# Kernel optimization log

Measured on AMD Instinct MI355X. Metric: run time of the kernel, lower is better.

The kernel has to match this reference:

```python
import jax, jax.numpy as jnp
import numpy as np

B, FMAX, H, LF, LC = 512, 16, 128, 64, 256
TAU, BIAS = 1000000.0, 1.0


def _gru(x, W_ih, W_hh, b_ih, b_hh):
    # x: [N, L, H]; torch GRU gate order (r, z, n)
    def step(h, xt):
        gi = xt @ W_ih.T + b_ih            # [N, 3H]
        gh = h @ W_hh.T + b_hh
        ir, iz, in_ = jnp.split(gi, 3, axis=-1)
        hr, hz, hn = jnp.split(gh, 3, axis=-1)
        r = jax.nn.sigmoid(ir + hr)
        z = jax.nn.sigmoid(iz + hz)
        n = jnp.tanh(in_ + r * hn)
        h_new = (1.0 - z) * n + z * h
        return h_new, h_new
    h0 = jnp.zeros((x.shape[0], W_hh.shape[1]), x.dtype)
    _, hs = jax.lax.scan(step, h0, jnp.swapaxes(x, 0, 1))
    return jnp.swapaxes(hs, 0, 1)          # [N, L, H]


def setup_inputs() -> dict:
    key = jax.random.key(0)
    ks = jax.random.split(key, 12)
    counts = (np.arange(B) % FMAX) + 1      # group sizes, max == FMAX
    N = int(counts.sum())                   # 4352
    user_idx = np.repeat(np.arange(B), counts).astype(np.int32)
    offsets = np.concatenate([[0], np.cumsum(counts)])
    gather_idx = np.zeros((B, FMAX), np.int32)
    pad_mask = np.zeros((B, FMAX), np.int32)
    for b in range(B):
        c = counts[b]
        gather_idx[b, :c] = offsets[b] + np.arange(c)
        pad_mask[b, :c] = 1
    lf = (np.arange(N) % LF) + 1
    friend_src_mask = (np.arange(LF)[None, :] < lf[:, None]).astype(np.int32)
    lc = (np.arange(N) % LC) + 1
    common_src_mask = (np.arange(LC)[None, :] < lc[:, None]).astype(np.int32)
    s = 1.0 / np.sqrt(H)
    return {
        "self_x": jax.random.normal(ks[0], (B, H), jnp.float32),
        "common_x": jax.random.normal(ks[1], (N, LC, H), jnp.float32),
        "common_time": jax.random.uniform(ks[2], (N, LC), jnp.float32) * 1e6,
        "friend_x": jax.random.normal(ks[3], (N, LF, H), jnp.float32),
        "W_ih": jax.random.uniform(ks[4], (3 * H, H), jnp.float32, -s, s),
        "W_hh": jax.random.uniform(ks[5], (3 * H, H), jnp.float32, -s, s),
        "b_ih": jax.random.uniform(ks[6], (3 * H,), jnp.float32, -s, s),
        "b_hh": jax.random.uniform(ks[7], (3 * H,), jnp.float32, -s, s),
        "W_friend": jax.random.uniform(ks[8], (H, 2 * H), jnp.float32, -s, s),
        "W_beta": jax.random.uniform(ks[9], (H, H), jnp.float32, -s, s),
        "friend_src_mask": jnp.asarray(friend_src_mask),
        "common_src_mask": jnp.asarray(common_src_mask),
        "user_idx": jnp.asarray(user_idx),
        "gather_idx": jnp.asarray(gather_idx),
        "pad_mask": jnp.asarray(pad_mask),
    }


def reference(self_x, common_x, common_time, friend_x, W_ih, W_hh, b_ih, b_hh,
              W_friend, W_beta, friend_src_mask, common_src_mask, user_idx,
              gather_idx, pad_mask):
    # --- FRIENDRNN: GRU encode, take last valid step per friend ---
    hs = _gru(friend_x, W_ih, W_hh, b_ih, b_hh)                 # [N, LF, H]
    fmask = friend_src_mask.astype(hs.dtype)
    hs = hs * fmask[..., None]
    idx_last = (friend_src_mask.sum(axis=1) - 1).astype(jnp.int32)  # [N]
    friend_out = jnp.take_along_axis(hs, idx_last[:, None, None], axis=1)[:, 0, :]  # [N, H]

    # --- FRIENDSHIP: temporal-decayed content attention over common items ---
    self_rep = self_x[user_idx]                                  # [N, H]
    sf = jnp.concatenate([self_rep, friend_out], axis=-1) @ W_friend.T  # [N, H]
    proj_common = common_x @ W_beta.T                            # [N, LC, H]
    scores = jnp.einsum('nlh,nh->nl', proj_common, sf)           # [N, LC]
    content = jax.nn.softplus(scores)
    temporal = jnp.exp(-common_time / TAU + BIAS)
    tf = jnp.sum(content * temporal * common_src_mask.astype(content.dtype), axis=-1)  # [N]

    # --- pad to groups (zeros, matching pad_sequence), softmax-weighted agg ---
    pm = pad_mask.astype(tf.dtype)                               # [B, FMAX]
    tf_pad = tf[gather_idx] * pm                                 # [B, FMAX]
    fx_pad = friend_out[gather_idx] * pm[..., None]              # [B, FMAX, H]
    w = jax.nn.softmax(tf_pad, axis=-1)                          # over padded zeros too (faithful)
    return jnp.sum(w[..., None] * fx_pad, axis=1)                # [B, H]
```

## Files before the change

kernel.cpp:

```cpp
#include <hip/hip_runtime.h>
#include <hip/hip_bf16.h>

typedef float float4v __attribute__((ext_vector_type(4)));
typedef __bf16 bf16x8 __attribute__((ext_vector_type(8)));

#define MFMA16(a, b, c) __builtin_amdgcn_mfma_f32_16x16x32_bf16(a, b, c, 0, 0, 0)

__device__ __forceinline__ float fsigmoid(float x) {
    return __builtin_amdgcn_rcpf(1.0f + __expf(-x));
}
__device__ __forceinline__ float ftanh_(float x) {
    float e = __expf(2.0f * x);
    return 1.0f - 2.0f * __builtin_amdgcn_rcpf(e + 1.0f);
}
__device__ __forceinline__ float softplusf(float x) {
    return fmaxf(x, 0.0f) + __logf(1.0f + __expf(-fabsf(x)));
}

__global__ __launch_bounds__(256, 1)
void gru_kernel(const float* __restrict__ friend_x,
                const float* __restrict__ W_ih, const float* __restrict__ W_hh,
                const float* __restrict__ b_ih, const float* __restrict__ b_hh,
                const int* __restrict__ fmask,
                float* __restrict__ friend_out)
{
    __shared__ __align__(16) __bf16 lds[8 * 2048];
    __shared__ int s_lf[16];
    __shared__ int s_n[16];

    const int tid = threadIdx.x;
    const int wv = tid >> 6;
    const int lane = tid & 63;
    const int cn = lane & 15;
    const int qq = lane >> 4;

    __bf16* const XH0 = lds;
    __bf16* const XH1 = lds + 2048;
    __bf16* const XL0 = lds + 2 * 2048;
    __bf16* const XL1 = lds + 3 * 2048;
    __bf16* const HH0 = lds + 4 * 2048;
    __bf16* const HH1 = lds + 5 * 2048;
    __bf16* const HL0 = lds + 6 * 2048;
    __bf16* const HL1 = lds + 7 * 2048;

    if (tid < 16) {
        const int p = blockIdx.x * 16 + tid;
        const int v = p / 68;
        const int j = p - v * 68;
        const int n = (63 - v) + 64 * j;
        s_n[tid] = n;
        const int* mp = fmask + (long)n * 64;
        int s = 0;
        for (int i = 0; i < 64; ++i) s += mp[i];
        s_lf[tid] = s;
    }

    {
        bf16x8 z8;
#pragma unroll
        for (int j = 0; j < 8; ++j) z8[j] = (__bf16)0.0f;
        for (int i = tid; i < 4 * 2048 / 8; i += 256) ((bf16x8*)HH0)[i] = z8;
    }

    bf16x8 wihh[3][2][4], wihl[3][2][4], whhh[3][2][4], whhl[3][2][4];
#pragma unroll
    for (int gate = 0; gate < 3; ++gate)
#pragma unroll
        for (int ct = 0; ct < 2; ++ct) {
            const int row = gate * 128 + wv * 32 + ct * 16 + cn;
#pragma unroll
            for (int c = 0; c < 4; ++c) {
                const float* p = W_ih + row * 128 + c * 32 + qq * 8;
                float4v u0 = *(const float4v*)p;
                float4v u1 = *(const float4v*)(p + 4);
                bf16x8 fh, fl;
#pragma unroll
                for (int j = 0; j < 4; ++j) {
                    __bf16 h0 = (__bf16)u0[j]; fh[j] = h0; fl[j] = (__bf16)(u0[j] - (float)h0);
                    __bf16 h1 = (__bf16)u1[j]; fh[j + 4] = h1; fl[j + 4] = (__bf16)(u1[j] - (float)h1);
                }
                wihh[gate][ct][c] = fh; wihl[gate][ct][c] = fl;
                const float* q = W_hh + row * 128 + c * 32 + qq * 8;
                float4v v0 = *(const float4v*)q;
                float4v v1 = *(const float4v*)(q + 4);
                bf16x8 gh, gl;
#pragma unroll
                for (int j = 0; j < 4; ++j) {
                    __bf16 h0 = (__bf16)v0[j]; gh[j] = h0; gl[j] = (__bf16)(v0[j] - (float)h0);
                    __bf16 h1 = (__bf16)v1[j]; gh[j + 4] = h1; gl[j + 4] = (__bf16)(v1[j] - (float)h1);
                }
                whhh[gate][ct][c] = gh; whhl[gate][ct][c] = gl;
            }
        }

    float biasR[2], biasZ[2], biasIN[2], biasHN[2];
#pragma unroll
    for (int ct = 0; ct < 2; ++ct) {
        const int cc = wv * 32 + ct * 16 + cn;
        biasR[ct] = b_ih[cc] + b_hh[cc];
        biasZ[ct] = b_ih[128 + cc] + b_hh[128 + cc];
        biasIN[ct] = b_ih[256 + cc];
        biasHN[ct] = b_hh[256 + cc];
    }

    __syncthreads();

    const int srow = lane & 15;
    const int ss = lane >> 4;
    const float* xp = friend_x + (long)s_n[srow] * 8192 + wv * 32 + ss * 8;

    int lfA[4], nA[4];
#pragma unroll
    for (int r = 0; r < 4; ++r) { lfA[r] = s_lf[qq * 4 + r]; nA[r] = s_n[qq * 4 + r]; }
    int maxlf = 0;
    for (int i = 0; i < 16; ++i) maxlf = (s_lf[i] > maxlf) ? s_lf[i] : maxlf;

    {
        float4v u0 = *(const float4v*)(xp);
        float4v u1 = *(const float4v*)(xp + 4);
        bf16x8 fh, fl;
#pragma unroll
        for (int j = 0; j < 4; ++j) {
            __bf16 h0 = (__bf16)u0[j]; fh[j] = h0; fl[j] = (__bf16)(u0[j] - (float)h0);
            __bf16 h1 = (__bf16)u1[j]; fh[j + 4] = h1; fl[j + 4] = (__bf16)(u1[j] - (float)h1);
        }
        *(bf16x8*)&XH0[tid * 8] = fh;
        *(bf16x8*)&XL0[tid * 8] = fl;
    }
    __syncthreads();

    float hC[2][4];
#pragma unroll
    for (int ct = 0; ct < 2; ++ct)
#pragma unroll
        for (int r = 0; r < 4; ++r) hC[ct][r] = 0.0f;

    for (int t = 0; t < maxlf; ++t) {
        const int cur = t & 1;
        __bf16* const XHc = cur ? XH1 : XH0;
        __bf16* const XLc = cur ? XL1 : XL0;
        __bf16* const HHc = cur ? HH1 : HH0;
        __bf16* const HLc = cur ? HL1 : HL0;
        __bf16* const XHn = cur ? XH0 : XH1;
        __bf16* const XLn = cur ? XL0 : XL1;
        __bf16* const HHn = cur ? HH0 : HH1;
        __bf16* const HLn = cur ? HL0 : HL1;
        const bool pf = (t + 1 < maxlf);

        float4v u0, u1;
        if (pf) {
            u0 = *(const float4v*)(xp + (t + 1) * 128);
            u1 = *(const float4v*)(xp + (t + 1) * 128 + 4);
        }

        float4v aR[2], aZ[2], aIN[2], aHN[2];
#pragma unroll
        for (int ct = 0; ct < 2; ++ct) {
            aR[ct] = (float4v){biasR[ct], biasR[ct], biasR[ct], biasR[ct]};
            aZ[ct] = (float4v){biasZ[ct], biasZ[ct], biasZ[ct], biasZ[ct]};
            aIN[ct] = (float4v){biasIN[ct], biasIN[ct], biasIN[ct], biasIN[ct]};
            aHN[ct] = (float4v){biasHN[ct], biasHN[ct], biasHN[ct], biasHN[ct]};
        }

#pragma unroll
        for (int c = 0; c < 4; ++c) {
            const int fo_ = (c * 64 + lane) * 8;
            bf16x8 xh = *(const bf16x8*)&XHc[fo_];
            bf16x8 xl = *(const bf16x8*)&XLc[fo_];
            bf16x8 hh = *(const bf16x8*)&HHc[fo_];
            bf16x8 hl = *(const bf16x8*)&HLc[fo_];
#pragma unroll
            for (int ct = 0; ct < 2; ++ct) {
                aR[ct] = MFMA16(xh, wihh[0][ct][c], aR[ct]);
                aR[ct] = MFMA16(xl, wihh[0][ct][c], aR[ct]);
                aR[ct] = MFMA16(xh, wihl[0][ct][c], aR[ct]);
                aR[ct] = MFMA16(hh, whhh[0][ct][c], aR[ct]);
                aR[ct] = MFMA16(hl, whhh[0][ct][c], aR[ct]);
                aR[ct] = MFMA16(hh, whhl[0][ct][c], aR[ct]);

                aZ[ct] = MFMA16(xh, wihh[1][ct][c], aZ[ct]);
                aZ[ct] = MFMA16(xl, wihh[1][ct][c], aZ[ct]);
                aZ[ct] = MFMA16(xh, wihl[1][ct][c], aZ[ct]);
                aZ[ct] = MFMA16(hh, whhh[1][ct][c], aZ[ct]);
                aZ[ct] = MFMA16(hl, whhh[1][ct][c], aZ[ct]);
                aZ[ct] = MFMA16(hh, whhl[1][ct][c], aZ[ct]);

                aIN[ct] = MFMA16(xh, wihh[2][ct][c], aIN[ct]);
                aIN[ct] = MFMA16(xl, wihh[2][ct][c], aIN[ct]);
                aIN[ct] = MFMA16(xh, wihl[2][ct][c], aIN[ct]);

                aHN[ct] = MFMA16(hh, whhh[2][ct][c], aHN[ct]);
                aHN[ct] = MFMA16(hl, whhh[2][ct][c], aHN[ct]);
                aHN[ct] = MFMA16(hh, whhl[2][ct][c], aHN[ct]);
            }
        }

#pragma unroll
        for (int ct = 0; ct < 2; ++ct) {
            const int col = wv * 32 + ct * 16 + cn;
            const int c2 = col >> 5, s2 = (col >> 3) & 3, j2 = col & 7;
#pragma unroll
            for (int reg = 0; reg < 4; ++reg) {
                const int row = qq * 4 + reg;
                float r = fsigmoid(aR[ct][reg]);
                float z = fsigmoid(aZ[ct][reg]);
                float nn = ftanh_(aIN[ct][reg] + r * aHN[ct][reg]);
                float h = (1.0f - z) * nn + z * hC[ct][reg];
                hC[ct][reg] = h;
                __bf16 hhi = (__bf16)h;
                __bf16 hlo = (__bf16)(h - (float)hhi);
                const int sl = (c2 * 64 + row + 16 * s2) * 8 + j2;
                HHn[sl] = hhi;
                HLn[sl] = hlo;
                if (t + 1 == lfA[reg])
                    friend_out[(long)nA[reg] * 128 + col] = h;
            }
        }

        if (pf) {
            bf16x8 fh, fl;
#pragma unroll
            for (int j = 0; j < 4; ++j) {
                __bf16 h0 = (__bf16)u0[j]; fh[j] = h0; fl[j] = (__bf16)(u0[j] - (float)h0);
                __bf16 h1 = (__bf16)u1[j]; fh[j + 4] = h1; fl[j + 4] = (__bf16)(u1[j] - (float)h1);
            }
            *(bf16x8*)&XHn[tid * 8] = fh;
            *(bf16x8*)&XLn[tid * 8] = fl;
        }
        __syncthreads();
    }
}

__global__ __launch_bounds__(256)
void attn_kernel(const float* __restrict__ self_x,
                 const float* __restrict__ common_x,
                 const float* __restrict__ common_time,
                 const float* __restrict__ W_friend,
                 const float* __restrict__ W_beta,
                 const int* __restrict__ csm,
                 const int* __restrict__ user_idx,
                 const float* __restrict__ friend_out,
                 float* __restrict__ tf)
{
    const int n = blockIdx.x;
    const int tid = threadIdx.x;
    const int wv = tid >> 6, lane = tid & 63;
    __shared__ __align__(16) float catf[256];
    __shared__ float sfs[128];
    __shared__ __align__(16) float vv[128];
    __shared__ float vpart[2][128];
    __shared__ int lcp[4];
    __shared__ int s_lc;
    __shared__ float wsum[4];

    if (tid < 128) catf[tid] = self_x[user_idx[n] * 128 + tid];
    else           catf[tid] = friend_out[(long)n * 128 + tid - 128];

    int mv = csm[(long)n * 256 + tid];
#pragma unroll
    for (int o = 32; o; o >>= 1) mv += __shfl_down(mv, o);
    if (lane == 0) lcp[wv] = mv;
    __syncthreads();
    if (tid == 0) s_lc = lcp[0] + lcp[1] + lcp[2] + lcp[3];

    float4v c4 = *(const float4v*)&catf[4 * lane];
    for (int i = 0; i < 32; ++i) {
        const int h = wv * 32 + i;
        float4v w4 = *(const float4v*)(W_friend + h * 256 + 4 * lane);
        float p = w4[0] * c4[0] + w4[1] * c4[1] + w4[2] * c4[2] + w4[3] * c4[3];
#pragma unroll
        for (int o = 1; o < 64; o <<= 1) p += __shfl_xor(p, o);
        if (lane == 0) sfs[h] = p;
    }
    __syncthreads();

    {
        const int col = tid & 127, half = tid >> 7;
        float acc = 0.f;
#pragma unroll 4
        for (int kk = 0; kk < 64; ++kk) {
            const int hh = kk * 2 + half;
            acc += sfs[hh] * W_beta[hh * 128 + col];
        }
        vpart[half][col] = acc;
    }
    __syncthreads();
    if (tid < 128) vv[tid] = vpart[0][tid] + vpart[1][tid];
    __syncthreads();

    const int lc = s_lc;
    const int lh = lane & 31, sub = lane >> 5;
    float4v v4 = *(const float4v*)&vv[4 * lh];
    const float* cxn = common_x + (long)n * 32768;
    const float* ctn = common_time + (long)n * 256;
    float acc = 0.f;
    for (int l0 = wv * 2 + sub; l0 < lc; l0 += 8) {
        float4v x4 = *(const float4v*)(cxn + l0 * 128 + 4 * lh);
        float p = x4[0] * v4[0] + x4[1] * v4[1] + x4[2] * v4[2] + x4[3] * v4[3];
#pragma unroll
        for (int o = 1; o < 32; o <<= 1) p += __shfl_xor(p, o);
        float contrib = softplusf(p) * __expf(1.0f - ctn[l0] * 1e-6f);
        if (lh == 0) acc += contrib;
    }
    acc += __shfl_xor(acc, 32);
    if (lane == 0) wsum[wv] = acc;
    __syncthreads();
    if (tid == 0) tf[n] = wsum[0] + wsum[1] + wsum[2] + wsum[3];
}

__global__ __launch_bounds__(128)
void agg_kernel(const float* __restrict__ tf, const float* __restrict__ fo,
                const int* __restrict__ gather_idx, const int* __restrict__ pad_mask,
                float* __restrict__ out)
{
    const int b = blockIdx.x, tid = threadIdx.x;
    __shared__ float tfp[16];
    __shared__ int gidx[16];
    __shared__ float pmf[16];
    if (tid < 16) {
        const int gg = gather_idx[b * 16 + tid];
        const int pp = pad_mask[b * 16 + tid];
        gidx[tid] = gg; pmf[tid] = (float)pp;
        tfp[tid] = pp ? tf[gg] : 0.0f;
    }
    __syncthreads();
    float m = tfp[0];
#pragma unroll
    for (int f = 1; f < 16; ++f) m = fmaxf(m, tfp[f]);
    float e[16]; float s = 0.f;
#pragma unroll
    for (int f = 0; f < 16; ++f) { e[f] = __expf(tfp[f] - m); s += e[f]; }
    const float inv = 1.0f / s;
    float acc = 0.f;
#pragma unroll
    for (int f = 0; f < 16; ++f) {
        if (pmf[f] != 0.0f) {
            const float w = e[f] * inv;
            acc += w * fo[(long)gidx[f] * 128 + tid];
        }
    }
    out[b * 128 + tid] = acc;
}

extern "C" void kernel_launch(void* const* d_in, const int* in_sizes, int n_in,
                              void* d_out, int out_size, void* d_ws, size_t ws_size,
                              hipStream_t stream)
{
    const float* self_x      = (const float*)d_in[0];
    const float* common_x    = (const float*)d_in[1];
    const float* common_time = (const float*)d_in[2];
    const float* friend_x    = (const float*)d_in[3];
    const float* W_ih        = (const float*)d_in[4];
    const float* W_hh        = (const float*)d_in[5];
    const float* b_ih        = (const float*)d_in[6];
    const float* b_hh        = (const float*)d_in[7];
    const float* W_friend    = (const float*)d_in[8];
    const float* W_beta      = (const float*)d_in[9];
    const int* fmask         = (const int*)d_in[10];
    const int* csm           = (const int*)d_in[11];
    const int* uidx          = (const int*)d_in[12];
    const int* gidx          = (const int*)d_in[13];
    const int* pmask         = (const int*)d_in[14];
    float* out = (float*)d_out;

    const int N = in_sizes[12];
    const int B = in_sizes[0] / 128;

    float* fo_ws = (float*)d_ws;
    float* tf_ws = fo_ws + (size_t)N * 128;

    gru_kernel<<<(N + 15) / 16, 256, 0, stream>>>(friend_x, W_ih, W_hh, b_ih, b_hh,
                                                  fmask, fo_ws);
    attn_kernel<<<N, 256, 0, stream>>>(self_x, common_x, common_time,
                                       W_friend, W_beta, csm, uidx, fo_ws, tf_ws);
    agg_kernel<<<B, 128, 0, stream>>>(tf_ws, fo_ws, gidx, pmask, out);

    (void)n_in; (void)out_size; (void)ws_size;
}
```

Before: 1.037 ms.

## Software-pipeline GRU input projection one step ahead and unroll attention loop

```diff
diff --git a/kernel.cpp b/kernel.cpp
--- a/kernel.cpp
+++ b/kernel.cpp
@@ -16,6 +16,47 @@
 __device__ __forceinline__ float softplusf(float x) {
     return fmaxf(x, 0.0f) + __logf(1.0f + __expf(-fabsf(x)));
 }
+
+#define STAGE(U0, U1, XHd, XLd) {                                              \
+    bf16x8 fh, fl;                                                             \
+    _Pragma("unroll")                                                          \
+    for (int j = 0; j < 4; ++j) {                                              \
+        __bf16 h0 = (__bf16)(U0)[j]; fh[j] = h0;                               \
+        fl[j] = (__bf16)((U0)[j] - (float)h0);                                 \
+        __bf16 h1 = (__bf16)(U1)[j]; fh[j + 4] = h1;                           \
+        fl[j + 4] = (__bf16)((U1)[j] - (float)h1);                             \
+    }                                                                          \
+    *(bf16x8*)&(XHd)[tid * 8] = fh;                                            \
+    *(bf16x8*)&(XLd)[tid * 8] = fl;                                            \
+}
+
+#define X_PHASE(XHp, XLp)                                                      \
+    _Pragma("unroll")                                                          \
+    for (int c = 0; c < 4; ++c) {                                              \
+        const int fo_ = (c * 64 + lane) * 8;                                   \
+        bf16x8 xh = *(const bf16x8*)&(XHp)[fo_];                               \
+        bf16x8 xl = *(const bf16x8*)&(XLp)[fo_];                               \
+        _Pragma("unroll")                                                      \
+        for (int ct = 0; ct < 2; ++ct) {                                       \
+            nR[ct]  = MFMA16(xh, wihh[0][ct][c], nR[ct]);                      \
+            nR[ct]  = MFMA16(xl, wihh[0][ct][c], nR[ct]);                      \
+            nR[ct]  = MFMA16(xh, wihl[0][ct][c], nR[ct]);                      \
+            nZ[ct]  = MFMA16(xh, wihh[1][ct][c], nZ[ct]);                      \
+            nZ[ct]  = MFMA16(xl, wihh[1][ct][c], nZ[ct]);                      \
+            nZ[ct]  = MFMA16(xh, wihl[1][ct][c], nZ[ct]);                      \
+            nIN[ct] = MFMA16(xh, wihh[2][ct][c], nIN[ct]);                     \
+            nIN[ct] = MFMA16(xl, wihh[2][ct][c], nIN[ct]);                     \
+            nIN[ct] = MFMA16(xh, wihl[2][ct][c], nIN[ct]);                     \
+        }                                                                      \
+    }
+
+#define NEXT_INIT()                                                            \
+    _Pragma("unroll")                                                          \
+    for (int ct = 0; ct < 2; ++ct) {                                           \
+        nR[ct]  = (float4v){biasR[ct],  biasR[ct],  biasR[ct],  biasR[ct]};    \
+        nZ[ct]  = (float4v){biasZ[ct],  biasZ[ct],  biasZ[ct],  biasZ[ct]};    \
+        nIN[ct] = (float4v){biasIN[ct], biasIN[ct], biasIN[ct], biasIN[ct]};   \
+    }
 
 __global__ __launch_bounds__(256, 1)
 void gru_kernel(const float* __restrict__ friend_x,
@@ -116,17 +157,18 @@
     for (int i = 0; i < 16; ++i) maxlf = (s_lf[i] > maxlf) ? s_lf[i] : maxlf;
 
     {
-        float4v u0 = *(const float4v*)(xp);
-        float4v u1 = *(const float4v*)(xp + 4);
-        bf16x8 fh, fl;
-#pragma unroll
-        for (int j = 0; j < 4; ++j) {
-            __bf16 h0 = (__bf16)u0[j]; fh[j] = h0; fl[j] = (__bf16)(u0[j] - (float)h0);
-            __bf16 h1 = (__bf16)u1[j]; fh[j + 4] = h1; fl[j + 4] = (__bf16)(u1[j] - (float)h1);
-        }
-        *(bf16x8*)&XH0[tid * 8] = fh;
-        *(bf16x8*)&XL0[tid * 8] = fl;
-    }
+        float4v a0 = *(const float4v*)(xp);
+        float4v a1 = *(const float4v*)(xp + 4);
+        float4v b0 = *(const float4v*)(xp + 128);
+        float4v b1 = *(const float4v*)(xp + 132);
+        STAGE(a0, a1, XH0, XL0);
+        STAGE(b0, b1, XH1, XL1);
+    }
+    __syncthreads();
+
+    float4v nR[2], nZ[2], nIN[2];
+    NEXT_INIT();
+    X_PHASE(XH0, XL0);
     __syncthreads();
 
     float hC[2][4];
@@ -137,62 +179,56 @@
 
     for (int t = 0; t < maxlf; ++t) {
         const int cur = t & 1;
-        __bf16* const XHc = cur ? XH1 : XH0;
-        __bf16* const XLc = cur ? XL1 : XL0;
         __bf16* const HHc = cur ? HH1 : HH0;
         __bf16* const HLc = cur ? HL1 : HL0;
-        __bf16* const XHn = cur ? XH0 : XH1;
-        __bf16* const XLn = cur ? XL0 : XL1;
+        __bf16* const XHr = cur ? XH0 : XH1;
+        __bf16* const XLr = cur ? XL0 : XL1;
+        __bf16* const XHw = cur ? XH1 : XH0;
+        __bf16* const XLw = cur ? XL1 : XL0;
         __bf16* const HHn = cur ? HH0 : HH1;
         __bf16* const HLn = cur ? HL0 : HL1;
-        const bool pf = (t + 1 < maxlf);
-
+
+        const bool pf2 = (t + 2 < maxlf);
         float4v u0, u1;
-        if (pf) {
-            u0 = *(const float4v*)(xp + (t + 1) * 128);
-            u1 = *(const float4v*)(xp + (t + 1) * 128 + 4);
+        if (pf2) {
+            u0 = *(const float4v*)(xp + (t + 2) * 128);
+            u1 = *(const float4v*)(xp + (t + 2) * 128 + 4);
         }
 
         float4v aR[2], aZ[2], aIN[2], aHN[2];
 #pragma unroll
         for (int ct = 0; ct < 2; ++ct) {
-            aR[ct] = (float4v){biasR[ct], biasR[ct], biasR[ct], biasR[ct]};
-            aZ[ct] = (float4v){biasZ[ct], biasZ[ct], biasZ[ct], biasZ[ct]};
-            aIN[ct] = (float4v){biasIN[ct], biasIN[ct], biasIN[ct], biasIN[ct]};
+            aR[ct] = nR[ct]; aZ[ct] = nZ[ct]; aIN[ct] = nIN[ct];
             aHN[ct] = (float4v){biasHN[ct], biasHN[ct], biasHN[ct], biasHN[ct]};
         }
 
 #pragma unroll
         for (int c = 0; c < 4; ++c) {
             const int fo_ = (c * 64 + lane) * 8;
-            bf16x8 xh = *(const bf16x8*)&XHc[fo_];
-            bf16x8 xl = *(const bf16x8*)&XLc[fo_];
             bf16x8 hh = *(const bf16x8*)&HHc[fo_];
             bf16x8 hl = *(const bf16x8*)&HLc[fo_];
 #pragma unroll
             for (int ct = 0; ct < 2; ++ct) {
-                aR[ct] = MFMA16(xh, wihh[0][ct][c], aR[ct]);
-                aR[ct] = MFMA16(xl, wihh[0][ct][c], aR[ct]);
-                aR[ct] = MFMA16(xh, wihl[0][ct][c], aR[ct]);
-                aR[ct] = MFMA16(hh, whhh[0][ct][c], aR[ct]);
-                aR[ct] = MFMA16(hl, whhh[0][ct][c], aR[ct]);
-                aR[ct] = MFMA16(hh, whhl[0][ct][c], aR[ct]);
-
-                aZ[ct] = MFMA16(xh, wihh[1][ct][c], aZ[ct]);
-                aZ[ct] = MFMA16(xl, wihh[1][ct][c], aZ[ct]);
-                aZ[ct] = MFMA16(xh, wihl[1][ct][c], aZ[ct]);
-                aZ[ct] = MFMA16(hh, whhh[1][ct][c], aZ[ct]);
-                aZ[ct] = MFMA16(hl, whhh[1][ct][c], aZ[ct]);
-                aZ[ct] = MFMA16(hh, whhl[1][ct][c], aZ[ct]);
-
-                aIN[ct] = MFMA16(xh, wihh[2][ct][c], aIN[ct]);
-                aIN[ct] = MFMA16(xl, wihh[2][ct][c], aIN[ct]);
-                aIN[ct] = MFMA16(xh, wihl[2][ct][c], aIN[ct]);
-
+                aR[ct]  = MFMA16(hh, whhh[0][ct][c], aR[ct]);
+                aR[ct]  = MFMA16(hl, whhh[0][ct][c], aR[ct]);
+                aR[ct]  = MFMA16(hh, whhl[0][ct][c], aR[ct]);
+                aZ[ct]  = MFMA16(hh, whhh[1][ct][c], aZ[ct]);
+                aZ[ct]  = MFMA16(hl, whhh[1][ct][c], aZ[ct]);
+                aZ[ct]  = MFMA16(hh, whhl[1][ct][c], aZ[ct]);
                 aHN[ct] = MFMA16(hh, whhh[2][ct][c], aHN[ct]);
                 aHN[ct] = MFMA16(hl, whhh[2][ct][c], aHN[ct]);
                 aHN[ct] = MFMA16(hh, whhl[2][ct][c], aHN[ct]);
             }
+        }
+
+        const bool hasNext = (t + 1 < maxlf);
+        if (hasNext) {
+            NEXT_INIT();
+            X_PHASE(XHr, XLr);
+        }
+
+        if (pf2) {
+            STAGE(u0, u1, XHw, XLw);
         }
 
 #pragma unroll
@@ -217,16 +253,6 @@
             }
         }
 
-        if (pf) {
-            bf16x8 fh, fl;
-#pragma unroll
-            for (int j = 0; j < 4; ++j) {
-                __bf16 h0 = (__bf16)u0[j]; fh[j] = h0; fl[j] = (__bf16)(u0[j] - (float)h0);
-                __bf16 h1 = (__bf16)u1[j]; fh[j + 4] = h1; fl[j + 4] = (__bf16)(u1[j] - (float)h1);
-            }
-            *(bf16x8*)&XHn[tid * 8] = fh;
-            *(bf16x8*)&XLn[tid * 8] = fl;
-        }
         __syncthreads();
     }
 }
@@ -291,11 +317,12 @@
     const int lc = s_lc;
     const int lh = lane & 31, sub = lane >> 5;
     float4v v4 = *(const float4v*)&vv[4 * lh];
-    const float* cxn = common_x + (long)n * 32768;
+    const float* cxn = common_x + (long)n * 32768 + 4 * lh;
     const float* ctn = common_time + (long)n * 256;
     float acc = 0.f;
+#pragma unroll 4
     for (int l0 = wv * 2 + sub; l0 < lc; l0 += 8) {
-        float4v x4 = *(const float4v*)(cxn + l0 * 128 + 4 * lh);
+        float4v x4 = *(const float4v*)(cxn + l0 * 128);
         float p = x4[0] * v4[0] + x4[1] * v4[1] + x4[2] * v4[2] + x4[3] * v4[3];
 #pragma unroll
         for (int o = 1; o < 32; o <<= 1) p += __shfl_xor(p, o);
```

After: 1.028 ms. No clear change (-0.9%).
